# Kernel optimization log

Measured on AMD Instinct MI355X. Metric: run time of the kernel, lower is better.

## Reference

```python
import jax, jax.numpy as jnp
import numpy as np
from jax import lax

B, N, F, HID = 32, 1000, 16, 64
HIST, FC = 24, 24
DEG = 16
E = B * N * DEG  # 512000 edges in block-diagonal batched graph
GC_IN = F + 2          # conv input: xn(1) + y(1) + X(F)
GRU_IN_ENC = GC_IN + HID


def setup_inputs() -> dict:
    key = jax.random.key(0)
    ks = jax.random.split(key, 24)
    X = jax.random.normal(ks[0], (B, HIST + FC, N, F), jnp.float32)
    y = jax.random.normal(ks[1], (B, HIST + FC, N, 1), jnp.float32)
    # edges stay within each batch's graph (dense_to_sparse of batch-repeated adj)
    src_local = jax.random.randint(ks[2], (B, N * DEG), 0, N)
    dst_local = jnp.tile(jnp.repeat(jnp.arange(N), DEG)[None, :], (B, 1))
    offs = (jnp.arange(B) * N)[:, None]
    edge_index = jnp.stack([(src_local + offs).reshape(-1),
                            (dst_local + offs).reshape(-1)], 0).astype(jnp.int32)
    edge_weight = jax.random.uniform(ks[3], (E,), jnp.float32)
    s = 0.1
    p = {
        'W_rel': s * jax.random.normal(ks[4], (GC_IN, HID), jnp.float32),
        'b_rel': jnp.zeros((HID,), jnp.float32),
        'W_root': s * jax.random.normal(ks[5], (GC_IN, HID), jnp.float32),
        'enc_Wih': s * jax.random.normal(ks[6], (3 * HID, GRU_IN_ENC), jnp.float32),
        'enc_Whh': s * jax.random.normal(ks[7], (3 * HID, HID), jnp.float32),
        'enc_bih': jnp.zeros((3 * HID,), jnp.float32),
        'enc_bhh': jnp.zeros((3 * HID,), jnp.float32),
        'enc_Wout': s * jax.random.normal(ks[8], (HID, 1), jnp.float32),
        'enc_bout': jnp.zeros((1,), jnp.float32),
        'dec_Win': s * jax.random.normal(ks[9], (4, HID), jnp.float32),
        'dec_bin': jnp.zeros((HID,), jnp.float32),
        'dec_Wih': s * jax.random.normal(ks[10], (3 * HID, HID), jnp.float32),
        'dec_Whh': s * jax.random.normal(ks[11], (3 * HID, HID), jnp.float32),
        'dec_bih': jnp.zeros((3 * HID,), jnp.float32),
        'dec_bhh': jnp.zeros((3 * HID,), jnp.float32),
        'dec_Wout': s * jax.random.normal(ks[12], (HID, 1), jnp.float32),
        'dec_bout': jnp.zeros((1,), jnp.float32),
    }
    return dict(X=X, y=y, edge_index=edge_index, edge_weight=edge_weight, **p)


def _gru_cell(x, h, Wih, Whh, bih, bhh):
    gi = x @ Wih.T + bih
    gh = h @ Whh.T + bhh
    ir, iz, inn = jnp.split(gi, 3, axis=-1)
    hr, hz, hnn = jnp.split(gh, 3, axis=-1)
    r = jax.nn.sigmoid(ir + hr)
    z = jax.nn.sigmoid(iz + hz)
    n = jnp.tanh(inn + r * hnn)
    return (1.0 - z) * n + z * h


def reference(X, y, edge_index, edge_weight,
              W_rel, b_rel, W_root,
              enc_Wih, enc_Whh, enc_bih, enc_bhh, enc_Wout, enc_bout,
              dec_Win, dec_bin, dec_Wih, dec_Whh, dec_bih, dec_bhh, dec_Wout, dec_bout):
    src, dst = edge_index[0], edge_index[1]

    def enc_step(carry, inp):
        hn, xn = carry          # hn: [B*N, HID], xn: [B, N, 1]
        X_t, y_t = inp          # [B,N,F], [B,N,1]
        x = jnp.concatenate([xn, y_t, X_t], axis=-1)   # [B,N,F+2]
        xg = x.reshape(B * N, GC_IN)
        msg = edge_weight[:, None] * xg[src]           # gather
        agg = jax.ops.segment_sum(msg, dst, num_segments=B * N)  # scatter-add
        conv = jax.nn.sigmoid(agg @ W_rel + b_rel + xg @ W_root)  # GraphConv
        xfull = jnp.concatenate([xg, conv], axis=-1)   # [B*N, F+2+HID]
        hn = _gru_cell(xfull, hn, enc_Wih, enc_Whh, enc_bih, enc_bhh)
        xn = hn.reshape(B, N, HID) @ enc_Wout + enc_bout
        return (hn, xn), None

    h0 = jnp.zeros((B * N, HID), X.dtype)
    xn0 = jnp.zeros((B, N, 1), X.dtype)
    X_enc = jnp.moveaxis(X[:, :HIST], 1, 0)   # [HIST,B,N,F]
    y_enc = jnp.moveaxis(y[:, :HIST], 1, 0)
    (hn, xn), _ = lax.scan(enc_step, (h0, xn0), (X_enc, y_enc))

    def dec_step(carry, X_t):
        hn, xn = carry
        x = jnp.concatenate([xn, X_t], axis=-1).reshape(B * N, 4)
        x = x @ dec_Win + dec_bin
        hn = _gru_cell(x, hn, dec_Wih, dec_Whh, dec_bih, dec_bhh)
        xn = hn.reshape(B, N, HID) @ dec_Wout + dec_bout
        return (hn, xn), xn

    X_dec = jnp.moveaxis(X[:, HIST:, :, -3:], 1, 0)  # [FC,B,N,3]
    _, preds = lax.scan(dec_step, (hn, xn), X_dec)
    return jnp.moveaxis(preds, 0, 1)                 # [B, FC, N, 1]
```

## Files before the change

### kernel.cpp

```cpp
#include <hip/hip_runtime.h>
#include <cstdint>

#define BX   32
#define NN   1000
#define FF   16
#define TT   48
#define HIST 24
#define FC   24
#define HID  64
#define DEG  16
#define BN   (BX*NN)
#define IMGP 40

typedef __attribute__((ext_vector_type(8)))  short s8v;
typedef __attribute__((ext_vector_type(16))) float f16v;

__device__ __forceinline__ float fastrcp(float d){
    float r = __builtin_amdgcn_rcpf(d);
    return r * (2.0f - d*r);
}
__device__ __forceinline__ float sigf(float x)  {
    return fastrcp(1.0f + __expf(-x));
}
__device__ __forceinline__ float tanhf_(float x){
    return 2.0f*fastrcp(1.0f + __expf(-2.0f*x)) - 1.0f;
}
__device__ __forceinline__ unsigned short f2bf(float x){
    unsigned int u = __float_as_uint(x);
    return (unsigned short)((u + 0x7FFFu + ((u>>16)&1u)) >> 16);
}
__device__ __forceinline__ float bf2f(unsigned short b){
    return __uint_as_float(((unsigned int)b)<<16);
}
__device__ __forceinline__ unsigned int cvtpk(float a, float b){
    unsigned int r;
    asm("v_cvt_pk_bf16_f32 %0, %1, %2" : "=v"(r) : "v"(a), "v"(b));
    return r;
}

__device__ __forceinline__ void  xn_st(float* p, float v){
    __hip_atomic_store(p, v, __ATOMIC_RELAXED, __HIP_MEMORY_SCOPE_AGENT);
}
__device__ __forceinline__ float xn_ld(const float* p){
    return __hip_atomic_load(p, __ATOMIC_RELAXED, __HIP_MEMORY_SCOPE_AGENT);
}

__device__ __forceinline__ void batch_barrier(unsigned int* bar, unsigned int target){
    __syncthreads();
    if (threadIdx.x == 0){
        asm volatile("s_waitcnt vmcnt(0)" ::: "memory");
        __hip_atomic_fetch_add(bar, 1u, __ATOMIC_RELAXED, __HIP_MEMORY_SCOPE_AGENT);
        while (__hip_atomic_load(bar, __ATOMIC_RELAXED, __HIP_MEMORY_SCOPE_AGENT) < target)
            __builtin_amdgcn_s_sleep(1);
    }
    __syncthreads();
}

__global__ void prep_weights(
    const float* __restrict__ W_rel, const float* __restrict__ W_root,
    const float* __restrict__ eWih, const float* __restrict__ eWhh,
    const float* __restrict__ dWih, const float* __restrict__ dWhh,
    unsigned short* __restrict__ encB, unsigned short* __restrict__ decB)
{
    const int i = blockIdx.x*256 + threadIdx.x;
    if (i < 64*56){
        int n = i/56, k = i%56;
        float v = 0.f;
        if (k < 17)                 v = W_rel[(k+1)*64 + n];
        else if (k == 17)           v = W_root[64 + n];
        else if (k >= 18 && k < 34) v = W_root[(k-16)*64 + n];
        else if (k == 34)           v = W_rel[n];
        else if (k == 35)           v = W_root[n];
        encB[i] = f2bf(v);
    }
    if (i < 192*96){
        int n = i/96, c = i%96;
        float v = 0.f;
        if (c >= 1 && c <= 17)       v = eWih[n*82 + c];
        else if (c == 19)            v = eWih[n*82 + 0];
        else if (c >= 32 && c < 96)  v = eWih[n*82 + 18 + (c-32)];
        encB[3584 + i] = f2bf(v);
    }
    if (i < 192*72){
        int n = i/72, k = i%72;
        encB[22016 + i] = f2bf((k < 64) ? eWhh[n*64 + k] : 0.f);
        decB[i]         = f2bf((k < 64) ? dWih[n*64 + k] : 0.f);
        decB[13824 + i] = f2bf((k < 64) ? dWhh[n*64 + k] : 0.f);
    }
}

__global__ __launch_bounds__(1024, 4) void agg_pre(
    const float* __restrict__ X, const float* __restrict__ y,
    const int*   __restrict__ esrc, const float* __restrict__ ew,
    unsigned short* __restrict__ img)
{
    extern __shared__ float sm[];
    float* Xs = sm;
    float* ys = sm + NN*FF;

    const int b = blockIdx.x;
    const int t = blockIdx.y;
    const float* Xt = X + (size_t)(b*TT + t)*NN*FF;
    const float* yt = y + (size_t)(b*TT + t)*NN;

    for (int i = threadIdx.x; i < NN*FF/4; i += 1024)
        ((float4*)Xs)[i] = ((const float4*)Xt)[i];
    for (int i = threadIdx.x; i < NN; i += 1024)
        ys[i] = yt[i];
    __syncthreads();

    const int nl = threadIdx.x;
    const int nc = (nl < NN) ? nl : NN-1;
    const int node = b*NN + nc;
    float a[18];
    #pragma unroll
    for (int i=0;i<17;i++) a[i]=0.f;
    const int4*   sv = (const int4*)  (esrc + node*DEG);
    const float4* wv = (const float4*)(ew   + node*DEG);
    #pragma unroll
    for (int q=0;q<4;q++){
        int4 s4 = sv[q]; float4 w4 = wv[q];
        const int   ss[4] = {s4.x, s4.y, s4.z, s4.w};
        const float ww[4] = {w4.x, w4.y, w4.z, w4.w};
        #pragma unroll
        for (int i=0;i<4;i++){
            const int sl = ss[i] - b*NN;
            const float wgt = ww[i];
            a[0] += wgt * ys[sl];
            const float4* sr = (const float4*)&Xs[sl*FF];
            #pragma unroll
            for (int q2=0;q2<4;q2++){
                float4 v = sr[q2];
                a[1+4*q2] += wgt*v.x; a[2+4*q2] += wgt*v.y;
                a[3+4*q2] += wgt*v.z; a[4+4*q2] += wgt*v.w;
            }
        }
    }
    a[17] = ys[nc];
    const int gblk = b*8 + (nl >> 7);
    unsigned int* w32 = (unsigned int*)(img +
        (((size_t)t*256 + gblk)*128 + (nl & 127))*IMGP);
    #pragma unroll
    for (int p=0;p<9;p++)  w32[p]   = cvtpk(a[2*p], a[2*p+1]);
    #pragma unroll
    for (int p=0;p<8;p++)  w32[9+p] = cvtpk(Xs[nc*FF+2*p], Xs[nc*FF+2*p+1]);
}

#define OFFB1   0
#define OFFBIH  3584
#define OFFBHH  22016
#define DOFFBIH 0
#define DOFFBHH 13824
#define OFFAS   35840
#define OFFAHB  53248
#define OFFHF   124928
#define FU_SMEM 159744
#define PAS  136
#define PB1  56
#define PBIH 96
#define PB72 72
#define PHF  68

__global__ __launch_bounds__(512, 1) void fused_steps(
    const float* __restrict__ X,
    const int* __restrict__ esrc, const float* __restrict__ ew,
    const unsigned short* __restrict__ img,
    const unsigned short* __restrict__ encB, const unsigned short* __restrict__ decB,
    const float* __restrict__ b_rel,
    const float* __restrict__ ebih, const float* __restrict__ ebhh,
    const float* __restrict__ eWout, const float* __restrict__ ebout,
    const float* __restrict__ dbih, const float* __restrict__ dbhh,
    const float* __restrict__ dWin, const float* __restrict__ dbin,
    const float* __restrict__ dWout, const float* __restrict__ dbout,
    float* __restrict__ xnA, float* __restrict__ xnB,
    unsigned int* __restrict__ bar, float* __restrict__ out)
{
    extern __shared__ char smraw[];
    __shared__ float xnL[128];
    unsigned short* sm16 = (unsigned short*)smraw;
    float* hf = (float*)(smraw + OFFHF);

    const int tid  = threadIdx.x;
    const int lane = tid & 63;
    const int w    = __builtin_amdgcn_readfirstlane(tid >> 6);
    const int mt = w >> 1, jt = w & 1;
    const int batch = blockIdx.x >> 3;
    const int sub   = blockIdx.x & 7;
    unsigned int* mybar = bar + batch*32;

    {
        const uint4* src = (const uint4*)encB;
        uint4* dst = (uint4*)smraw;
        for (int i = tid; i < 4480; i += 512) dst[i] = src[i];
        unsigned int* z32 = (unsigned int*)(smraw + 71680);
        for (int i = tid; i < 22016; i += 512) z32[i] = 0u;
    }

    f16v hreg = {};
    int4 esv0={0,0,0,0}, esv1={0,0,0,0}, esv2={0,0,0,0}, esv3={0,0,0,0};
    float4 ewv0={}, ewv1={}, ewv2={}, ewv3={};
    int g_node = 0;
    if (tid < 128){
        const int nl2 = sub*128 + tid;
        const int nc  = (nl2 < NN) ? nl2 : NN-1;
        g_node = batch*NN + nc;
        const int4*   sv = (const int4*)  (esrc + g_node*DEG);
        const float4* wv = (const float4*)(ew   + g_node*DEG);
        esv0=sv[0]; esv1=sv[1]; esv2=sv[2]; esv3=sv[3];
        ewv0=wv[0]; ewv1=wv[1]; ewv2=wv[2]; ewv3=wv[3];
    }
    __syncthreads();

    {
        const unsigned short* imgrow = img + (((size_t)0*256 + blockIdx.x)*128)*IMGP;
        {
            int node = tid >> 2, part = tid & 3;
            uint4 v = *(const uint4*)(imgrow + node*IMGP + part*8);
            *(uint4*)(sm16 + OFFAS + node*PAS + part*8) = v;
        }
        if (tid < 128){
            unsigned int v = *(const unsigned int*)(imgrow + tid*IMGP + 32);
            *(unsigned int*)(sm16 + OFFAS + tid*PAS + 32) = v;
        }
    }

    for (int t = 0; t < TT; ++t){
        const bool enc = (t < HIST);
        const float* xn_r = (t & 1) ? xnB : xnA;
        float*       xn_w = (t & 1) ? xnA : xnB;

        if (enc){
            if (tid < 128){
                float a0 = 0.f, xnv = 0.f;
                if (t > 0){
                    a0 += ewv0.x*xn_ld(xn_r + esv0.x) + ewv0.y*xn_ld(xn_r + esv0.y)
                        + ewv0.z*xn_ld(xn_r + esv0.z) + ewv0.w*xn_ld(xn_r + esv0.w);
                    a0 += ewv1.x*xn_ld(xn_r + esv1.x) + ewv1.y*xn_ld(xn_r + esv1.y)
                        + ewv1.z*xn_ld(xn_r + esv1.z) + ewv1.w*xn_ld(xn_r + esv1.w);
                    a0 += ewv2.x*xn_ld(xn_r + esv2.x) + ewv2.y*xn_ld(xn_r + esv2.y)
                        + ewv2.z*xn_ld(xn_r + esv2.z) + ewv2.w*xn_ld(xn_r + esv2.w);
                    a0 += ewv3.x*xn_ld(xn_r + esv3.x) + ewv3.y*xn_ld(xn_r + esv3.y)
                        + ewv3.z*xn_ld(xn_r + esv3.z) + ewv3.w*xn_ld(xn_r + esv3.w);
                    xnv = xn_ld(xn_r + g_node);
                }
                *(unsigned int*)(sm16 + OFFAS + tid*PAS + 34) = cvtpk(a0, xnv);
            }
            __syncthreads();

            {
                f16v acc = {};
                const int rA = mt*32 + (lane & 31);
                const int rB = jt*32 + (lane & 31);
                const int ke = (lane >> 5)*8;
                #pragma unroll
                for (int ks=0; ks<3; ks++){
                    s8v a = *(const s8v*)(sm16 + OFFAS + rA*PAS + ks*16 + ke);
                    s8v b = *(const s8v*)(sm16 + OFFB1 + rB*PB1 + ks*16 + ke);
                    acc = __builtin_amdgcn_mfma_f32_32x32x16_bf16(a, b, acc, 0, 0, 0);
                }
                const int j = jt*32 + (lane & 31);
                const float brl = b_rel[j];
                #pragma unroll
                for (int p=0; p<8; p++){
                    float s0 = sigf(acc[2*p]   + brl);
                    float s1 = sigf(acc[2*p+1] + brl);
                    unsigned int pk = cvtpk(s0, s1);
                    int row = ((2*p)&3) + 8*(p>>1) + 4*(lane>>5);
                    sm16[OFFAS + (mt*32 + row  )*PAS + 64 + j] = (unsigned short)pk;
                    sm16[OFFAS + (mt*32 + row+1)*PAS + 64 + j] = (unsigned short)(pk>>16);
                }
            }
            __syncthreads();

            f16v accx[3] = {{},{},{}};
            f16v acch[3] = {{},{},{}};
            {
                const int rA = mt*32 + (lane & 31);
                const int ln = lane & 31;
                const int ke = (lane >> 5)*8;
                #pragma unroll
                for (int s=0; s<6; s++){
                    const int acol = (s < 2) ? (16 + 16*s) : (32 + 16*s);
                    s8v a = *(const s8v*)(sm16 + OFFAS + rA*PAS + acol + ke);
                    #pragma unroll
                    for (int nt=0; nt<3; nt++){
                        int NT = jt + nt*2;
                        s8v b = *(const s8v*)(sm16 + OFFBIH + (NT*32 + ln)*PBIH + s*16 + ke);
                        accx[nt] = __builtin_amdgcn_mfma_f32_32x32x16_bf16(a, b, accx[nt], 0,0,0);
                    }
                }
                #pragma unroll
                for (int ks=0; ks<4; ks++){
                    s8v ah = *(const s8v*)(sm16 + OFFAHB + rA*PB72 + ks*16 + ke);
                    #pragma unroll
                    for (int nt=0; nt<3; nt++){
                        int NT = jt + nt*2;
                        s8v b = *(const s8v*)(sm16 + OFFBHH + (NT*32 + ln)*PB72 + ks*16 + ke);
                        acch[nt] = __builtin_amdgcn_mfma_f32_32x32x16_bf16(ah, b, acch[nt], 0,0,0);
                    }
                }
            }
            __syncthreads();

            {
                const int j = jt*32 + (lane & 31);
                const float br  = ebih[j]     + ebhh[j];
                const float bz  = ebih[64+j]  + ebhh[64+j];
                const float bin_ = ebih[128+j];
                const float bhn  = ebhh[128+j];
                #pragma unroll
                for (int p=0; p<8; p++){
                    const int r0 = 2*p, r1 = 2*p+1;
                    int row = ((r0)&3) + 8*(p>>1) + 4*(lane>>5);
                    const int n0 = mt*32 + row, n1 = n0 + 1;
                    float hold0 = hreg[r0];
                    float hold1 = hreg[r1];
                    float rr0 = sigf(accx[0][r0] + acch[0][r0] + br);
                    float rr1 = sigf(accx[0][r1] + acch[0][r1] + br);
                    float zz0 = sigf(accx[1][r0] + acch[1][r0] + bz);
                    float zz1 = sigf(accx[1][r1] + acch[1][r1] + bz);
                    float nn0 = tanhf_(accx[2][r0] + bin_ + rr0*(acch[2][r0] + bhn));
                    float nn1 = tanhf_(accx[2][r1] + bin_ + rr1*(acch[2][r1] + bhn));
                    float hp0 = (1.f - zz0)*nn0 + zz0*hold0;
                    float hp1 = (1.f - zz1)*nn1 + zz1*hold1;
                    hreg[r0] = hp0;
                    hreg[r1] = hp1;
                    hf[n0*PHF + j] = hp0;
                    hf[n1*PHF + j] = hp1;
                    unsigned int nh = cvtpk(hp0, hp1);
                    sm16[OFFAHB + n0*PB72 + j] = (unsigned short)nh;
                    sm16[OFFAHB + n1*PB72 + j] = (unsigned short)(nh>>16);
                }
            }
            __syncthreads();

            if (t+1 < HIST){
                const unsigned short* imgrow = img +
                    (((size_t)(t+1)*256 + blockIdx.x)*128)*IMGP;
                {
                    int node = tid >> 2, part = tid & 3;
                    uint4 v = *(const uint4*)(imgrow + node*IMGP + part*8);
                    *(uint4*)(sm16 + OFFAS + node*PAS + part*8) = v;
                }
                if (tid < 128){
                    unsigned int v = *(const unsigned int*)(imgrow + tid*IMGP + 32);
                    *(unsigned int*)(sm16 + OFFAS + tid*PAS + 32) = v;
                }
            }

            if (tid < 128){
                const float4* hv = (const float4*)(hf + tid*PHF);
                float s = ebout[0];
                #pragma unroll
                for (int q=0; q<16; q++){
                    float4 v = hv[q];
                    s += v.x*eWout[4*q] + v.y*eWout[4*q+1]
                       + v.z*eWout[4*q+2] + v.w*eWout[4*q+3];
                }
                const int nl2 = sub*128 + tid;
                if (nl2 < NN) xn_st(xn_w + batch*NN + nl2, s);
            }
        } else {
            if (t == HIST){
                const uint4* src = (const uint4*)decB;
                uint4* dst = (uint4*)smraw;
                for (int i = tid; i < 3456; i += 512) dst[i] = src[i];
            }
            {
                const int node = tid >> 2, c0 = (tid & 3)*16;
                const int nl2 = sub*128 + node;
                const int nc  = (nl2 < NN) ? nl2 : NN-1;
                const float* Xt = X + (size_t)(batch*TT + t)*NN*FF;
                float x0 = (t == HIST) ? xn_ld(xn_r + batch*NN + nc) : xnL[node];
                float x1 = Xt[nc*FF + 13];
                float x2 = Xt[nc*FF + 14];
                float x3 = Xt[nc*FF + 15];
                unsigned int* ax32 = (unsigned int*)(sm16 + OFFAS);
                #pragma unroll
                for (int p=0; p<8; p++){
                    int c = c0 + 2*p;
                    float va = dbin[c]   + x0*dWin[c]     + x1*dWin[64+c]   + x2*dWin[128+c]   + x3*dWin[192+c];
                    float vb = dbin[c+1] + x0*dWin[c+1]   + x1*dWin[64+c+1] + x2*dWin[128+c+1] + x3*dWin[192+c+1];
                    ax32[(node*PB72 + c) >> 1] = cvtpk(va, vb);
                }
            }
            __syncthreads();

            f16v accx[3] = {{},{},{}};
            f16v acch[3] = {{},{},{}};
            {
                const int rA = mt*32 + (lane & 31);
                const int ln = lane & 31;
                const int ke = (lane >> 5)*8;
                #pragma unroll
                for (int ks=0; ks<4; ks++){
                    s8v a = *(const s8v*)(sm16 + OFFAS + rA*PB72 + ks*16 + ke);
                    #pragma unroll
                    for (int nt=0; nt<3; nt++){
                        int NT = jt + nt*2;
                        s8v b = *(const s8v*)(sm16 + DOFFBIH + (NT*32 + ln)*PB72 + ks*16 + ke);
                        accx[nt] = __builtin_amdgcn_mfma_f32_32x32x16_bf16(a, b, accx[nt], 0,0,0);
                    }
                }
                #pragma unroll
                for (int ks=0; ks<4; ks++){
                    s8v ah = *(const s8v*)(sm16 + OFFAHB + rA*PB72 + ks*16 + ke);
                    #pragma unroll
                    for (int nt=0; nt<3; nt++){
                        int NT = jt + nt*2;
                        s8v b = *(const s8v*)(sm16 + DOFFBHH + (NT*32 + ln)*PB72 + ks*16 + ke);
                        acch[nt] = __builtin_amdgcn_mfma_f32_32x32x16_bf16(ah, b, acch[nt], 0,0,0);
                    }
                }
            }
            __syncthreads();

            {
                const int j = jt*32 + (lane & 31);
                const float br  = dbih[j]     + dbhh[j];
                const float bz  = dbih[64+j]  + dbhh[64+j];
                const float bin_ = dbih[128+j];
                const float bhn  = dbhh[128+j];
                #pragma unroll
                for (int p=0; p<8; p++){
                    const int r0 = 2*p, r1 = 2*p+1;
                    int row = ((r0)&3) + 8*(p>>1) + 4*(lane>>5);
                    const int n0 = mt*32 + row, n1 = n0 + 1;
                    float hold0 = hreg[r0];
                    float hold1 = hreg[r1];
                    float rr0 = sigf(accx[0][r0] + acch[0][r0] + br);
                    float rr1 = sigf(accx[0][r1] + acch[0][r1] + br);
                    float zz0 = sigf(accx[1][r0] + acch[1][r0] + bz);
                    float zz1 = sigf(accx[1][r1] + acch[1][r1] + bz);
                    float nn0 = tanhf_(accx[2][r0] + bin_ + rr0*(acch[2][r0] + bhn));
                    float nn1 = tanhf_(accx[2][r1] + bin_ + rr1*(acch[2][r1] + bhn));
                    float hp0 = (1.f - zz0)*nn0 + zz0*hold0;
                    float hp1 = (1.f - zz1)*nn1 + zz1*hold1;
                    hreg[r0] = hp0;
                    hreg[r1] = hp1;
                    hf[n0*PHF + j] = hp0;
                    hf[n1*PHF + j] = hp1;
                    unsigned int nh = cvtpk(hp0, hp1);
                    sm16[OFFAHB + n0*PB72 + j] = (unsigned short)nh;
                    sm16[OFFAHB + n1*PB72 + j] = (unsigned short)(nh>>16);
                }
            }
            __syncthreads();

            if (tid < 128){
                const float4* hv = (const float4*)(hf + tid*PHF);
                float s = dbout[0];
                #pragma unroll
                for (int q=0; q<16; q++){
                    float4 v = hv[q];
                    s += v.x*dWout[4*q] + v.y*dWout[4*q+1]
                       + v.z*dWout[4*q+2] + v.w*dWout[4*q+3];
                }
                xnL[tid] = s;
                const int nl2 = sub*128 + tid;
                if (nl2 < NN)
                    out[(size_t)(batch*FC + (t - HIST))*NN + nl2] = s;
            }
        }
        if (t < HIST-1) batch_barrier(mybar, 8u*(unsigned)(t+1));
        else            __syncthreads();
    }
}

extern "C" void kernel_launch(void* const* d_in, const int* in_sizes, int n_in,
                              void* d_out, int out_size, void* d_ws, size_t ws_size,
                              hipStream_t stream)
{
    const float* X     = (const float*)d_in[0];
    const float* y     = (const float*)d_in[1];
    const int*   ei    = (const int*)  d_in[2];
    const float* ew    = (const float*)d_in[3];
    const float* W_rel = (const float*)d_in[4];
    const float* b_rel = (const float*)d_in[5];
    const float* W_root= (const float*)d_in[6];
    const float* eWih  = (const float*)d_in[7];
    const float* eWhh  = (const float*)d_in[8];
    const float* ebih  = (const float*)d_in[9];
    const float* ebhh  = (const float*)d_in[10];
    const float* eWout = (const float*)d_in[11];
    const float* ebout = (const float*)d_in[12];
    const float* dWin  = (const float*)d_in[13];
    const float* dbin  = (const float*)d_in[14];
    const float* dWih  = (const float*)d_in[15];
    const float* dWhh  = (const float*)d_in[16];
    const float* dbih  = (const float*)d_in[17];
    const float* dbhh  = (const float*)d_in[18];
    const float* dWout = (const float*)d_in[19];
    const float* dbout = (const float*)d_in[20];
    float* out = (float*)d_out;

    unsigned short* img = (unsigned short*)d_ws;
    float* x0 = (float*)(img + (size_t)24*256*128*IMGP);
    float* x1 = x0 + BN;
    unsigned short* encB = (unsigned short*)(x1 + BN);
    unsigned short* decB = encB + 35840;
    unsigned int* bar = (unsigned int*)(decB + 27648);

    const int* esrc = ei;

    const int smA = (NN*FF + NN)*sizeof(float);
    hipFuncSetAttribute((const void*)agg_pre,
                        hipFuncAttributeMaxDynamicSharedMemorySize, smA);
    hipFuncSetAttribute((const void*)fused_steps,
                        hipFuncAttributeMaxDynamicSharedMemorySize, FU_SMEM);

    hipMemsetAsync(bar, 0, 32*32*sizeof(unsigned int), stream);
    prep_weights<<<78, 256, 0, stream>>>(W_rel, W_root, eWih, eWhh, dWih, dWhh, encB, decB);
    agg_pre<<<dim3(BX,24), 1024, smA, stream>>>(X, y, esrc, ew, img);

    void* args[] = {
        (void*)&X, (void*)&esrc, (void*)&ew, (void*)&img,
        (void*)&encB, (void*)&decB,
        (void*)&b_rel, (void*)&ebih, (void*)&ebhh, (void*)&eWout, (void*)&ebout,
        (void*)&dbih, (void*)&dbhh, (void*)&dWin, (void*)&dbin, (void*)&dWout, (void*)&dbout,
        (void*)&x0, (void*)&x1, (void*)&bar, (void*)&out
    };
    hipLaunchCooperativeKernel((const void*)fused_steps, dim3(256), dim3(512),
                               args, FU_SMEM, stream);
}
```

Measured before the change: 414.9 us.

## Overlap neighbor gather with first conv MFMAs and prefetch next-step image earlier

The encoder step now issues all sixteen neighbor xn loads up front and runs the first two K-slices of the graph-conv MFMA, which only touch columns already in shared memory, before the aggregate is written. Only the last K-slice, which holds the aggregate and xn columns, stays after the barrier. The load of the next timestep's input image moves before the GRU gate epilogue so its global latency overlaps that math. This aims to hide gather and global-load latency in the serial recurrence, at the cost of more live registers and a dependence on the next image not overwriting columns still being read.

```diff
diff --git a/kernel.cpp b/kernel.cpp
--- a/kernel.cpp
+++ b/kernel.cpp
@@ -230,34 +230,49 @@
         float*       xn_w = (t & 1) ? xnA : xnB;
 
         if (enc){
+            const int rA = mt*32 + (lane & 31);
+            const int rB = jt*32 + (lane & 31);
+            const int ke = (lane >> 5)*8;
+
+            float xl0=0,xl1=0,xl2=0,xl3=0,xl4=0,xl5=0,xl6=0,xl7=0;
+            float xl8=0,xl9=0,xl10=0,xl11=0,xl12=0,xl13=0,xl14=0,xl15=0;
+            float xnv = 0.f;
+            if (tid < 128 && t > 0){
+                xl0 = xn_ld(xn_r + esv0.x); xl1 = xn_ld(xn_r + esv0.y);
+                xl2 = xn_ld(xn_r + esv0.z); xl3 = xn_ld(xn_r + esv0.w);
+                xl4 = xn_ld(xn_r + esv1.x); xl5 = xn_ld(xn_r + esv1.y);
+                xl6 = xn_ld(xn_r + esv1.z); xl7 = xn_ld(xn_r + esv1.w);
+                xl8 = xn_ld(xn_r + esv2.x); xl9 = xn_ld(xn_r + esv2.y);
+                xl10= xn_ld(xn_r + esv2.z); xl11= xn_ld(xn_r + esv2.w);
+                xl12= xn_ld(xn_r + esv3.x); xl13= xn_ld(xn_r + esv3.y);
+                xl14= xn_ld(xn_r + esv3.z); xl15= xn_ld(xn_r + esv3.w);
+                xnv = xn_ld(xn_r + g_node);
+            }
+
+            f16v acc = {};
+            #pragma unroll
+            for (int ks=0; ks<2; ks++){
+                s8v a = *(const s8v*)(sm16 + OFFAS + rA*PAS + ks*16 + ke);
+                s8v b = *(const s8v*)(sm16 + OFFB1 + rB*PB1 + ks*16 + ke);
+                acc = __builtin_amdgcn_mfma_f32_32x32x16_bf16(a, b, acc, 0, 0, 0);
+            }
+
             if (tid < 128){
-                float a0 = 0.f, xnv = 0.f;
+                float a0 = 0.f;
                 if (t > 0){
-                    a0 += ewv0.x*xn_ld(xn_r + esv0.x) + ewv0.y*xn_ld(xn_r + esv0.y)
-                        + ewv0.z*xn_ld(xn_r + esv0.z) + ewv0.w*xn_ld(xn_r + esv0.w);
-                    a0 += ewv1.x*xn_ld(xn_r + esv1.x) + ewv1.y*xn_ld(xn_r + esv1.y)
-                        + ewv1.z*xn_ld(xn_r + esv1.z) + ewv1.w*xn_ld(xn_r + esv1.w);
-                    a0 += ewv2.x*xn_ld(xn_r + esv2.x) + ewv2.y*xn_ld(xn_r + esv2.y)
-                        + ewv2.z*xn_ld(xn_r + esv2.z) + ewv2.w*xn_ld(xn_r + esv2.w);
-                    a0 += ewv3.x*xn_ld(xn_r + esv3.x) + ewv3.y*xn_ld(xn_r + esv3.y)
-                        + ewv3.z*xn_ld(xn_r + esv3.z) + ewv3.w*xn_ld(xn_r + esv3.w);
-                    xnv = xn_ld(xn_r + g_node);
+                    a0  = ewv0.x*xl0 + ewv0.y*xl1 + ewv0.z*xl2 + ewv0.w*xl3;
+                    a0 += ewv1.x*xl4 + ewv1.y*xl5 + ewv1.z*xl6 + ewv1.w*xl7;
+                    a0 += ewv2.x*xl8 + ewv2.y*xl9 + ewv2.z*xl10 + ewv2.w*xl11;
+                    a0 += ewv3.x*xl12 + ewv3.y*xl13 + ewv3.z*xl14 + ewv3.w*xl15;
                 }
                 *(unsigned int*)(sm16 + OFFAS + tid*PAS + 34) = cvtpk(a0, xnv);
             }
             __syncthreads();
 
             {
-                f16v acc = {};
-                const int rA = mt*32 + (lane & 31);
-                const int rB = jt*32 + (lane & 31);
-                const int ke = (lane >> 5)*8;
-                #pragma unroll
-                for (int ks=0; ks<3; ks++){
-                    s8v a = *(const s8v*)(sm16 + OFFAS + rA*PAS + ks*16 + ke);
-                    s8v b = *(const s8v*)(sm16 + OFFB1 + rB*PB1 + ks*16 + ke);
-                    acc = __builtin_amdgcn_mfma_f32_32x32x16_bf16(a, b, acc, 0, 0, 0);
-                }
+                s8v a = *(const s8v*)(sm16 + OFFAS + rA*PAS + 32 + ke);
+                s8v b = *(const s8v*)(sm16 + OFFB1 + rB*PB1 + 32 + ke);
+                acc = __builtin_amdgcn_mfma_f32_32x32x16_bf16(a, b, acc, 0, 0, 0);
                 const int j = jt*32 + (lane & 31);
                 const float brl = b_rel[j];
                 #pragma unroll
@@ -275,9 +290,7 @@
             f16v accx[3] = {{},{},{}};
             f16v acch[3] = {{},{},{}};
             {
-                const int rA = mt*32 + (lane & 31);
                 const int ln = lane & 31;
-                const int ke = (lane >> 5)*8;
                 #pragma unroll
                 for (int s=0; s<6; s++){
                     const int acol = (s < 2) ? (16 + 16*s) : (32 + 16*s);
@@ -301,6 +314,20 @@
                 }
             }
             __syncthreads();
+
+            if (t+1 < HIST){
+                const unsigned short* imgrow = img +
+                    (((size_t)(t+1)*256 + blockIdx.x)*128)*IMGP;
+                {
+                    int node = tid >> 2, part = tid & 3;
+                    uint4 v = *(const uint4*)(imgrow + node*IMGP + part*8);
+                    *(uint4*)(sm16 + OFFAS + node*PAS + part*8) = v;
+                }
+                if (tid < 128){
+                    unsigned int v = *(const unsigned int*)(imgrow + tid*IMGP + 32);
+                    *(unsigned int*)(sm16 + OFFAS + tid*PAS + 32) = v;
+                }
+            }
 
             {
                 const int j = jt*32 + (lane & 31);
@@ -333,20 +360,6 @@
                 }
             }
             __syncthreads();
-
-            if (t+1 < HIST){
-                const unsigned short* imgrow = img +
-                    (((size_t)(t+1)*256 + blockIdx.x)*128)*IMGP;
-                {
-                    int node = tid >> 2, part = tid & 3;
-                    uint4 v = *(const uint4*)(imgrow + node*IMGP + part*8);
-                    *(uint4*)(sm16 + OFFAS + node*PAS + part*8) = v;
-                }
-                if (tid < 128){
-                    unsigned int v = *(const unsigned int*)(imgrow + tid*IMGP + 32);
-                    *(unsigned int*)(sm16 + OFFAS + tid*PAS + 32) = v;
-                }
-            }
 
             if (tid < 128){
                 const float4* hv = (const float4*)(hf + tid*PHF);
```

Measured after the change: 412.0 us. Within noise of the previous version (-0.7%).
